# Kernel optimization log

Measured on AMD Instinct MI355X. Metric: run time of the kernel, lower is better.

## Reference

```python
import jax, jax.numpy as jnp
import numpy as np

TWO_PI = 2.0 * np.pi
DIST_THRESH = 0.1  # squared-distance threshold from the source


def _fourier_basis(x, y, K):
    # phase[i, l, k] = 2*pi*(k*x_i + l*y_i), k,l in 1..K, reshaped to [inchans, K*K]
    kk = jnp.arange(1, K + 1, dtype=x.dtype)  # varies along last axis (columns)
    ll = jnp.arange(1, K + 1, dtype=x.dtype)  # varies along middle axis (rows)
    phase = TWO_PI * (kk[None, None, :] * x[:, None, None]
                      + ll[None, :, None] * y[:, None, None])
    phase = phase.reshape(x.shape[0], K * K)
    return jnp.cos(phase), jnp.sin(phase)


def setup_inputs() -> dict:
    key = jax.random.key(0)
    ks = jax.random.split(key, 7)
    B, C_in, C_out, K, T = 128, 273, 270, 32, 2048
    return {
        "X": jax.random.normal(ks[0], (B, C_in, T), dtype=jnp.float32),
        "z_real": jax.random.normal(ks[1], (C_out, K * K), dtype=jnp.float32) / (32.0 * 32.0),
        "z_imag": jax.random.normal(ks[2], (C_out, K * K), dtype=jnp.float32) / (32.0 * 32.0),
        "x": jax.random.uniform(ks[3], (C_in,), dtype=jnp.float32),
        "y": jax.random.uniform(ks[4], (C_in,), dtype=jnp.float32),
        "x_drop": jax.random.uniform(ks[5], (), dtype=jnp.float32),
        "y_drop": jax.random.uniform(ks[6], (), dtype=jnp.float32),
    }


def reference(X, z_real, z_imag, x, y, x_drop, y_drop):
    K = int(np.sqrt(z_real.shape[1]))
    cos_m, sin_m = _fourier_basis(x, y, K)          # [C_in, K*K] each
    # logits over input channels: [C_out, C_in]
    a = z_real @ cos_m.T + z_imag @ sin_m.T
    # zero (not -inf) logits of channels near the drop point, as in the source
    dist2 = (x_drop - x) ** 2 + (y_drop - y) ** 2   # [C_in]
    a = jnp.where((dist2 < DIST_THRESH)[None, :], 0.0, a)
    a = jax.nn.softmax(a, axis=1)                    # [C_out, C_in]
    return jnp.einsum('oi,bit->bot', a, X)           # [B, C_out, T]
```

## Files before the change

kernel.cpp:

```cpp
#include <hip/hip_runtime.h>
#include <hip/hip_bf16.h>
#include <math.h>

typedef short s16x4 __attribute__((ext_vector_type(4)));
typedef short bf16x8 __attribute__((ext_vector_type(8)));
typedef float f32x16 __attribute__((ext_vector_type(16)));

#define C_IN 273
#define C_OUT 270
#define T_DIM 2048
#define KP 288
#define NKS 18

#define XT_KS_STRIDE 65536u
#define XT_PER_B 1179648u
#define WS2_COS   150994944u
#define WS2_SIN   152113152u
#define WS2_PART  153231360u
#define WS2_APERM 155738112u
#define APR2_KS_STRIDE 9216u

#define TR_ROW 4104
#define TR_LDS (16 * TR_ROW)

__device__ __forceinline__ short f2bf(float f) {
  __hip_bfloat16 h = __float2bfloat16(f);
  short r; __builtin_memcpy(&r, &h, 2); return r;
}

__global__ void k_basis(const float* __restrict__ x, const float* __restrict__ y,
                        float* __restrict__ cosb, float* __restrict__ sinb) {
  const int i = blockIdx.x;
  const float xi = x[i], yi = y[i];
  const int base = threadIdx.x * 4;
  #pragma unroll
  for (int j = 0; j < 4; ++j) {
    const int kl = base + j;
    const float kf = (float)((kl & 31) + 1);
    const float lf = (float)((kl >> 5) + 1);
    const float ph = 6.28318530717958647692f * (kf * xi + lf * yi);
    float sn, cs;
    sincosf(ph, &sn, &cs);
    cosb[(size_t)i * 1024 + kl] = cs;
    sinb[(size_t)i * 1024 + kl] = sn;
  }
}

__global__ __launch_bounds__(256) void k_logits(const float* __restrict__ zr,
    const float* __restrict__ zi, const float* __restrict__ cosb,
    const float* __restrict__ sinb, float* __restrict__ part) {
  const int tx = threadIdx.x & 15, ty = threadIdx.x >> 4;
  const int ibase = blockIdx.x * 64 + tx * 4;
  const int obase = blockIdx.y * 64 + ty * 4;
  const int kl0 = (int)blockIdx.z * 128;
  int oc[4], ic[4];
  #pragma unroll
  for (int a = 0; a < 4; ++a) {
    oc[a] = min(obase + a, C_OUT - 1);
    ic[a] = min(ibase + a, C_IN - 1);
  }
  float acc[4][4] = {};
  for (int kl = kl0; kl < kl0 + 128; kl += 4) {
    float4 zr4[4], zi4[4], cb4[4], sb4[4];
    #pragma unroll
    for (int a = 0; a < 4; ++a) {
      zr4[a] = *(const float4*)(zr + (size_t)oc[a] * 1024 + kl);
      zi4[a] = *(const float4*)(zi + (size_t)oc[a] * 1024 + kl);
    }
    #pragma unroll
    for (int b = 0; b < 4; ++b) {
      cb4[b] = *(const float4*)(cosb + (size_t)ic[b] * 1024 + kl);
      sb4[b] = *(const float4*)(sinb + (size_t)ic[b] * 1024 + kl);
    }
    #pragma unroll
    for (int a = 0; a < 4; ++a)
      #pragma unroll
      for (int b = 0; b < 4; ++b)
        acc[a][b] += zr4[a].x * cb4[b].x + zr4[a].y * cb4[b].y
                   + zr4[a].z * cb4[b].z + zr4[a].w * cb4[b].w
                   + zi4[a].x * sb4[b].x + zi4[a].y * sb4[b].y
                   + zi4[a].z * sb4[b].z + zi4[a].w * sb4[b].w;
  }
  #pragma unroll
  for (int a = 0; a < 4; ++a)
    #pragma unroll
    for (int b = 0; b < 4; ++b) {
      const int o = obase + a, i = ibase + b;
      if (o < C_OUT && i < C_IN)
        part[((size_t)blockIdx.z * 272 + o) * 288 + i] = acc[a][b];
    }
}

__global__ __launch_bounds__(256) void k_softmax(const float* __restrict__ part,
    const float* __restrict__ x, const float* __restrict__ y,
    const float* __restrict__ xdp, const float* __restrict__ ydp,
    __hip_bfloat16* __restrict__ ap2) {
  const int o = blockIdx.x;
  const int tid = threadIdx.x;
  if (o >= C_OUT) {
    for (int s = tid; s < KP; s += 256)
      ap2[(size_t)((s >> 4) * 288 + o) * 16 + (s & 15)] = __float2bfloat16(0.f);
    return;
  }
  __shared__ float red[8];
  const float xd = xdp[0], yd = ydp[0];
  const int i0 = tid, i1 = tid + 256;
  float v0, v1 = 0.f;
  {
    float s = 0.f;
    #pragma unroll
    for (int c = 0; c < 8; ++c) s += part[((size_t)c * 272 + o) * 288 + i0];
    const float dx = xd - x[i0], dy = yd - y[i0];
    v0 = (dx * dx + dy * dy < 0.1f) ? 0.f : s;
  }
  const bool has1 = (i1 < C_IN);
  if (has1) {
    float s = 0.f;
    #pragma unroll
    for (int c = 0; c < 8; ++c) s += part[((size_t)c * 272 + o) * 288 + i1];
    const float dx = xd - x[i1], dy = yd - y[i1];
    v1 = (dx * dx + dy * dy < 0.1f) ? 0.f : s;
  }
  float mv = has1 ? fmaxf(v0, v1) : v0;
  #pragma unroll
  for (int off = 32; off >= 1; off >>= 1) mv = fmaxf(mv, __shfl_down(mv, off));
  if ((tid & 63) == 0) red[tid >> 6] = mv;
  __syncthreads();
  const float M = fmaxf(fmaxf(red[0], red[1]), fmaxf(red[2], red[3]));
  const float e0 = expf(v0 - M);
  const float e1 = has1 ? expf(v1 - M) : 0.f;
  float sv = e0 + e1;
  #pragma unroll
  for (int off = 32; off >= 1; off >>= 1) sv += __shfl_down(sv, off);
  __syncthreads();
  if ((tid & 63) == 0) red[4 + (tid >> 6)] = sv;
  __syncthreads();
  const float S = red[4] + red[5] + red[6] + red[7];
  const float inv = 1.0f / S;
  ap2[(size_t)((i0 >> 4) * 288 + o) * 16 + (i0 & 15)] = __float2bfloat16(e0 * inv);
  if (i1 < KP)
    ap2[(size_t)((i1 >> 4) * 288 + o) * 16 + (i1 & 15)] =
        __float2bfloat16(has1 ? e1 * inv : 0.f);
}

__global__ __launch_bounds__(256) void k_trans(const float* __restrict__ X,
                                               char* __restrict__ Xt) {
  __shared__ __align__(16) char lds[TR_LDS];
  const int tid = threadIdx.x;
  const int ks = blockIdx.x;
  const int b  = blockIdx.y;
  const float* Xb = X + (size_t)b * C_IN * T_DIM;

  const int ri = tid >> 4;
  const int tq = tid & 15;
  const int gi = ks * 16 + ri;
  const bool valid = (gi < C_IN);
  const float* src = Xb + (size_t)gi * T_DIM + tq * 4;
  char* ldsrow = lds + ri * TR_ROW + tq * 8;

  #pragma unroll 8
  for (int p = 0; p < 32; ++p) {
    float4 v = valid ? *(const float4*)(src + p * 64) : make_float4(0.f, 0.f, 0.f, 0.f);
    s16x4 pk;
    pk[0] = f2bf(v.x); pk[1] = f2bf(v.y); pk[2] = f2bf(v.z); pk[3] = f2bf(v.w);
    *(s16x4*)(ldsrow + p * 128) = pk;
  }
  __syncthreads();

  char* dstB = Xt + (size_t)b * XT_PER_B + (size_t)ks * XT_KS_STRIDE;
  #pragma unroll
  for (int it = 0; it < 16; ++it) {
    const int u = it * 256 + tid;
    const int t = u >> 1, half = (u & 1) * 8;
    unsigned short w[8];
    #pragma unroll
    for (int r = 0; r < 8; ++r)
      w[r] = *(const unsigned short*)(lds + (half + r) * TR_ROW + t * 2);
    uint4 pk;
    pk.x = (unsigned)w[0] | ((unsigned)w[1] << 16);
    pk.y = (unsigned)w[2] | ((unsigned)w[3] << 16);
    pk.z = (unsigned)w[4] | ((unsigned)w[5] << 16);
    pk.w = (unsigned)w[6] | ((unsigned)w[7] << 16);
    *(uint4*)(dstB + (size_t)u * 16) = pk;
  }
}

__global__ __launch_bounds__(256) void k_gemm3(const __hip_bfloat16* __restrict__ ap2,
    const char* __restrict__ Xt, float* __restrict__ out) {
  const int tid = threadIdx.x;
  const int lane = tid & 63, w = tid >> 6;
  const int l32 = lane & 31, lh = lane >> 5;
  const int bid = blockIdx.x;
  const int L = (bid & 7) * 768 + (bid >> 3);
  const int ob = L % 3;
  const int rest = L / 3;
  const int tb = rest & 15;
  const int b  = rest >> 4;

  const int tblk = tb * 4 + w;
  const char* Bbase = Xt + (size_t)b * XT_PER_B + tblk * 1024 + l32 * 32 + lh * 16;
  const char* Abase = (const char*)ap2 + (ob * 96 + l32) * 32 + lh * 16;

  f32x16 acc[3] = {};
  bf16x8 Bf[3], Af[3][3];

  Bf[0]    = *(const bf16x8*)(Bbase);
  Af[0][0] = *(const bf16x8*)(Abase);
  Af[0][1] = *(const bf16x8*)(Abase + 1024);
  Af[0][2] = *(const bf16x8*)(Abase + 2048);
  Bf[1]    = *(const bf16x8*)(Bbase + XT_KS_STRIDE);
  Af[1][0] = *(const bf16x8*)(Abase + APR2_KS_STRIDE);
  Af[1][1] = *(const bf16x8*)(Abase + APR2_KS_STRIDE + 1024);
  Af[1][2] = *(const bf16x8*)(Abase + APR2_KS_STRIDE + 2048);
  __builtin_amdgcn_sched_barrier(0);

  #pragma unroll
  for (int ks = 0; ks < NKS; ++ks) {
    const int cur = ks % 3;
    if (ks + 2 < NKS) {
      const int nxt = (ks + 2) % 3;
      Bf[nxt]    = *(const bf16x8*)(Bbase + (size_t)(ks + 2) * XT_KS_STRIDE);
      Af[nxt][0] = *(const bf16x8*)(Abase + (ks + 2) * APR2_KS_STRIDE);
      Af[nxt][1] = *(const bf16x8*)(Abase + (ks + 2) * APR2_KS_STRIDE + 1024);
      Af[nxt][2] = *(const bf16x8*)(Abase + (ks + 2) * APR2_KS_STRIDE + 2048);
    }
    __builtin_amdgcn_sched_barrier(0);
    acc[0] = __builtin_amdgcn_mfma_f32_32x32x16_bf16(Af[cur][0], Bf[cur], acc[0], 0, 0, 0);
    acc[1] = __builtin_amdgcn_mfma_f32_32x32x16_bf16(Af[cur][1], Bf[cur], acc[1], 0, 0, 0);
    acc[2] = __builtin_amdgcn_mfma_f32_32x32x16_bf16(Af[cur][2], Bf[cur], acc[2], 0, 0, 0);
    __builtin_amdgcn_sched_barrier(0);
  }

  const int t = tblk * 32 + l32;
  float* outb = out + (size_t)b * C_OUT * T_DIM;
  #pragma unroll
  for (int mi = 0; mi < 3; ++mi)
    #pragma unroll
    for (int r = 0; r < 16; ++r) {
      const int o = ob * 96 + mi * 32 + (r & 3) + 8 * (r >> 2) + 4 * lh;
      if (o < C_OUT)
        outb[(size_t)o * T_DIM + t] = acc[mi][r];
    }
}

extern "C" void kernel_launch(void* const* d_in, const int* in_sizes, int n_in,
                              void* d_out, int out_size, void* d_ws, size_t ws_size,
                              hipStream_t stream) {
  const float* X  = (const float*)d_in[0];
  const float* zr = (const float*)d_in[1];
  const float* zi = (const float*)d_in[2];
  const float* x  = (const float*)d_in[3];
  const float* y  = (const float*)d_in[4];
  const float* xd = (const float*)d_in[5];
  const float* yd = (const float*)d_in[6];
  float* out = (float*)d_out;
  char* ws = (char*)d_ws;

  float* cosb = (float*)(ws + WS2_COS);
  float* sinb = (float*)(ws + WS2_SIN);
  float* part = (float*)(ws + WS2_PART);
  __hip_bfloat16* ap2 = (__hip_bfloat16*)(ws + WS2_APERM);
  char* Xt = ws;

  k_basis<<<dim3(273), dim3(256), 0, stream>>>(x, y, cosb, sinb);
  k_logits<<<dim3(5, 5, 8), dim3(256), 0, stream>>>(zr, zi, cosb, sinb, part);
  k_softmax<<<dim3(KP), dim3(256), 0, stream>>>(part, x, y, xd, yd, ap2);
  k_trans<<<dim3(18, 128), dim3(256), 0, stream>>>(X, Xt);
  k_gemm3<<<dim3(6144), dim3(256), 0, stream>>>(ap2, Xt, out);
}
```

Measured before the change: 348.6 us.

## Widen GEMM tile to two time blocks per wave and relayout transposed X

The main GEMM kernel now has each wave compute two 32-wide time blocks, so each A fragment load is reused across two MFMAs and the grid shrinks from 6144 to 3072 blocks. The transposed X buffer is relaid out so the K-slices of one time group sit contiguously, which makes the B loads over successive K steps sequential. A is now double-buffered while B stays triple-buffered. The logits kernel also moves to smaller 2x2 per-thread tiles on a 9x9x8 grid to spread that small stage over more blocks. In exchange, the GEMM uses more accumulator registers, which may lower occupancy.

```diff
diff --git a/kernel.cpp b/kernel.cpp
--- a/kernel.cpp
+++ b/kernel.cpp
@@ -12,7 +12,7 @@
 #define KP 288
 #define NKS 18
 
-#define XT_KS_STRIDE 65536u
+#define XT_G_STRIDE 18432u
 #define XT_PER_B 1179648u
 #define WS2_COS   150994944u
 #define WS2_SIN   152113152u
@@ -50,41 +50,41 @@
     const float* __restrict__ zi, const float* __restrict__ cosb,
     const float* __restrict__ sinb, float* __restrict__ part) {
   const int tx = threadIdx.x & 15, ty = threadIdx.x >> 4;
-  const int ibase = blockIdx.x * 64 + tx * 4;
-  const int obase = blockIdx.y * 64 + ty * 4;
+  const int ibase = blockIdx.x * 32 + tx * 2;
+  const int obase = blockIdx.y * 32 + ty * 2;
   const int kl0 = (int)blockIdx.z * 128;
-  int oc[4], ic[4];
-  #pragma unroll
-  for (int a = 0; a < 4; ++a) {
+  int oc[2], ic[2];
+  #pragma unroll
+  for (int a = 0; a < 2; ++a) {
     oc[a] = min(obase + a, C_OUT - 1);
     ic[a] = min(ibase + a, C_IN - 1);
   }
-  float acc[4][4] = {};
+  float acc[2][2] = {};
   for (int kl = kl0; kl < kl0 + 128; kl += 4) {
-    float4 zr4[4], zi4[4], cb4[4], sb4[4];
-    #pragma unroll
-    for (int a = 0; a < 4; ++a) {
+    float4 zr4[2], zi4[2], cb4[2], sb4[2];
+    #pragma unroll
+    for (int a = 0; a < 2; ++a) {
       zr4[a] = *(const float4*)(zr + (size_t)oc[a] * 1024 + kl);
       zi4[a] = *(const float4*)(zi + (size_t)oc[a] * 1024 + kl);
     }
     #pragma unroll
-    for (int b = 0; b < 4; ++b) {
+    for (int b = 0; b < 2; ++b) {
       cb4[b] = *(const float4*)(cosb + (size_t)ic[b] * 1024 + kl);
       sb4[b] = *(const float4*)(sinb + (size_t)ic[b] * 1024 + kl);
     }
     #pragma unroll
-    for (int a = 0; a < 4; ++a)
+    for (int a = 0; a < 2; ++a)
       #pragma unroll
-      for (int b = 0; b < 4; ++b)
+      for (int b = 0; b < 2; ++b)
         acc[a][b] += zr4[a].x * cb4[b].x + zr4[a].y * cb4[b].y
                    + zr4[a].z * cb4[b].z + zr4[a].w * cb4[b].w
                    + zi4[a].x * sb4[b].x + zi4[a].y * sb4[b].y
                    + zi4[a].z * sb4[b].z + zi4[a].w * sb4[b].w;
   }
   #pragma unroll
-  for (int a = 0; a < 4; ++a)
-    #pragma unroll
-    for (int b = 0; b < 4; ++b) {
+  for (int a = 0; a < 2; ++a)
+    #pragma unroll
+    for (int b = 0; b < 2; ++b) {
       const int o = obase + a, i = ibase + b;
       if (o < C_OUT && i < C_IN)
         part[((size_t)blockIdx.z * 272 + o) * 288 + i] = acc[a][b];
@@ -167,11 +167,12 @@
   }
   __syncthreads();
 
-  char* dstB = Xt + (size_t)b * XT_PER_B + (size_t)ks * XT_KS_STRIDE;
+  char* dstB = Xt + (size_t)b * XT_PER_B + (size_t)ks * 1024u;
   #pragma unroll
   for (int it = 0; it < 16; ++it) {
     const int u = it * 256 + tid;
     const int t = u >> 1, half = (u & 1) * 8;
+    const int g = t >> 5, tg = t & 31;
     unsigned short w[8];
     #pragma unroll
     for (int r = 0; r < 8; ++r)
@@ -181,65 +182,75 @@
     pk.y = (unsigned)w[2] | ((unsigned)w[3] << 16);
     pk.z = (unsigned)w[4] | ((unsigned)w[5] << 16);
     pk.w = (unsigned)w[6] | ((unsigned)w[7] << 16);
-    *(uint4*)(dstB + (size_t)u * 16) = pk;
-  }
-}
-
-__global__ __launch_bounds__(256) void k_gemm3(const __hip_bfloat16* __restrict__ ap2,
+    *(uint4*)(dstB + (size_t)g * XT_G_STRIDE + tg * 32 + half * 2) = pk;
+  }
+}
+
+__global__ __launch_bounds__(256) void k_gemm4(const __hip_bfloat16* __restrict__ ap2,
     const char* __restrict__ Xt, float* __restrict__ out) {
   const int tid = threadIdx.x;
   const int lane = tid & 63, w = tid >> 6;
   const int l32 = lane & 31, lh = lane >> 5;
   const int bid = blockIdx.x;
-  const int L = (bid & 7) * 768 + (bid >> 3);
+  const int L = (bid & 7) * 384 + (bid >> 3);
   const int ob = L % 3;
   const int rest = L / 3;
-  const int tb = rest & 15;
-  const int b  = rest >> 4;
-
-  const int tblk = tb * 4 + w;
-  const char* Bbase = Xt + (size_t)b * XT_PER_B + tblk * 1024 + l32 * 32 + lh * 16;
-  const char* Abase = (const char*)ap2 + (ob * 96 + l32) * 32 + lh * 16;
-
-  f32x16 acc[3] = {};
-  bf16x8 Bf[3], Af[3][3];
-
-  Bf[0]    = *(const bf16x8*)(Bbase);
-  Af[0][0] = *(const bf16x8*)(Abase);
-  Af[0][1] = *(const bf16x8*)(Abase + 1024);
-  Af[0][2] = *(const bf16x8*)(Abase + 2048);
-  Bf[1]    = *(const bf16x8*)(Bbase + XT_KS_STRIDE);
-  Af[1][0] = *(const bf16x8*)(Abase + APR2_KS_STRIDE);
-  Af[1][1] = *(const bf16x8*)(Abase + APR2_KS_STRIDE + 1024);
-  Af[1][2] = *(const bf16x8*)(Abase + APR2_KS_STRIDE + 2048);
+  const int tb = rest & 7;
+  const int b  = rest >> 3;
+
+  const int g0 = tb * 8 + w * 2;
+  const char* Bb0 = Xt + (size_t)b * XT_PER_B + (size_t)g0 * XT_G_STRIDE + l32 * 32 + lh * 16;
+  const char* Bb1 = Bb0 + XT_G_STRIDE;
+  const char* Ab  = (const char*)ap2 + (ob * 96 + l32) * 32 + lh * 16;
+
+  f32x16 acc[3][2] = {};
+  bf16x8 Bf[3][2], Af[2][3];
+
+  Bf[0][0] = *(const bf16x8*)(Bb0);
+  Bf[0][1] = *(const bf16x8*)(Bb1);
+  Bf[1][0] = *(const bf16x8*)(Bb0 + 1024);
+  Bf[1][1] = *(const bf16x8*)(Bb1 + 1024);
+  Af[0][0] = *(const bf16x8*)(Ab);
+  Af[0][1] = *(const bf16x8*)(Ab + 1024);
+  Af[0][2] = *(const bf16x8*)(Ab + 2048);
   __builtin_amdgcn_sched_barrier(0);
 
   #pragma unroll
   for (int ks = 0; ks < NKS; ++ks) {
-    const int cur = ks % 3;
+    const int c3 = ks % 3, c2 = ks % 2;
     if (ks + 2 < NKS) {
-      const int nxt = (ks + 2) % 3;
-      Bf[nxt]    = *(const bf16x8*)(Bbase + (size_t)(ks + 2) * XT_KS_STRIDE);
-      Af[nxt][0] = *(const bf16x8*)(Abase + (ks + 2) * APR2_KS_STRIDE);
-      Af[nxt][1] = *(const bf16x8*)(Abase + (ks + 2) * APR2_KS_STRIDE + 1024);
-      Af[nxt][2] = *(const bf16x8*)(Abase + (ks + 2) * APR2_KS_STRIDE + 2048);
+      const int n3 = (ks + 2) % 3;
+      Bf[n3][0] = *(const bf16x8*)(Bb0 + (ks + 2) * 1024);
+      Bf[n3][1] = *(const bf16x8*)(Bb1 + (ks + 2) * 1024);
+    }
+    if (ks + 1 < NKS) {
+      const int n2 = (ks + 1) % 2;
+      Af[n2][0] = *(const bf16x8*)(Ab + (ks + 1) * APR2_KS_STRIDE);
+      Af[n2][1] = *(const bf16x8*)(Ab + (ks + 1) * APR2_KS_STRIDE + 1024);
+      Af[n2][2] = *(const bf16x8*)(Ab + (ks + 1) * APR2_KS_STRIDE + 2048);
     }
     __builtin_amdgcn_sched_barrier(0);
-    acc[0] = __builtin_amdgcn_mfma_f32_32x32x16_bf16(Af[cur][0], Bf[cur], acc[0], 0, 0, 0);
-    acc[1] = __builtin_amdgcn_mfma_f32_32x32x16_bf16(Af[cur][1], Bf[cur], acc[1], 0, 0, 0);
-    acc[2] = __builtin_amdgcn_mfma_f32_32x32x16_bf16(Af[cur][2], Bf[cur], acc[2], 0, 0, 0);
+    acc[0][0] = __builtin_amdgcn_mfma_f32_32x32x16_bf16(Af[c2][0], Bf[c3][0], acc[0][0], 0, 0, 0);
+    acc[0][1] = __builtin_amdgcn_mfma_f32_32x32x16_bf16(Af[c2][0], Bf[c3][1], acc[0][1], 0, 0, 0);
+    acc[1][0] = __builtin_amdgcn_mfma_f32_32x32x16_bf16(Af[c2][1], Bf[c3][0], acc[1][0], 0, 0, 0);
+    acc[1][1] = __builtin_amdgcn_mfma_f32_32x32x16_bf16(Af[c2][1], Bf[c3][1], acc[1][1], 0, 0, 0);
+    acc[2][0] = __builtin_amdgcn_mfma_f32_32x32x16_bf16(Af[c2][2], Bf[c3][0], acc[2][0], 0, 0, 0);
+    acc[2][1] = __builtin_amdgcn_mfma_f32_32x32x16_bf16(Af[c2][2], Bf[c3][1], acc[2][1], 0, 0, 0);
     __builtin_amdgcn_sched_barrier(0);
   }
 
-  const int t = tblk * 32 + l32;
   float* outb = out + (size_t)b * C_OUT * T_DIM;
   #pragma unroll
   for (int mi = 0; mi < 3; ++mi)
     #pragma unroll
-    for (int r = 0; r < 16; ++r) {
-      const int o = ob * 96 + mi * 32 + (r & 3) + 8 * (r >> 2) + 4 * lh;
-      if (o < C_OUT)
-        outb[(size_t)o * T_DIM + t] = acc[mi][r];
+    for (int n = 0; n < 2; ++n) {
+      const int t = (g0 + n) * 32 + l32;
+      #pragma unroll
+      for (int r = 0; r < 16; ++r) {
+        const int o = ob * 96 + mi * 32 + (r & 3) + 8 * (r >> 2) + 4 * lh;
+        if (o < C_OUT)
+          outb[(size_t)o * T_DIM + t] = acc[mi][n][r];
+      }
     }
 }
 
@@ -263,8 +274,8 @@
   char* Xt = ws;
 
   k_basis<<<dim3(273), dim3(256), 0, stream>>>(x, y, cosb, sinb);
-  k_logits<<<dim3(5, 5, 8), dim3(256), 0, stream>>>(zr, zi, cosb, sinb, part);
+  k_logits<<<dim3(9, 9, 8), dim3(256), 0, stream>>>(zr, zi, cosb, sinb, part);
   k_softmax<<<dim3(KP), dim3(256), 0, stream>>>(part, x, y, xd, yd, ap2);
   k_trans<<<dim3(18, 128), dim3(256), 0, stream>>>(X, Xt);
-  k_gemm3<<<dim3(6144), dim3(256), 0, stream>>>(ap2, Xt, out);
-}
+  k_gemm4<<<dim3(3072), dim3(256), 0, stream>>>(ap2, Xt, out);
+}
```

New measurement: 324.6 us. -6.9%, faster.
